# Performance work log

Hardware: AMD Instinct MI355X
Metric: run time of the kernel (lower is better)

The kernel has to match this reference:

```python
import jax, jax.numpy as jnp
import numpy as np

MARGIN = 0.3


def setup_inputs() -> dict:
    key = jax.random.key(0)
    k1, k2 = jax.random.split(key)
    N, D = 8192, 128
    embeddings = jax.random.normal(k1, (N, D), dtype=jnp.float32)
    labels = jax.random.randint(k2, (N,), 0, 512, dtype=jnp.int64)
    return {"embeddings": embeddings, "labels": labels}


def _pairwise_dist(x):
    # Euclidean cdist via squared-norm expansion; safe sqrt (zero grad at d==0).
    sq_norms = jnp.sum(x * x, axis=-1)  # [N]
    sq = sq_norms[:, None] + sq_norms[None, :] - 2.0 * (x @ x.T)  # [N, N]
    sq = jnp.maximum(sq, 0.0)
    safe = jnp.where(sq > 0.0, sq, 1.0)
    return jnp.where(sq > 0.0, jnp.sqrt(safe), 0.0)


def reference(embeddings, labels):
    d = _pairwise_dist(embeddings)  # [N, N]
    same = labels[:, None] == labels[None, :]
    eye = jnp.eye(labels.shape[0], dtype=bool)
    pos_mask = same & ~eye
    neg_mask = ~same

    inf = jnp.float32(jnp.inf)
    hardest_pos = jnp.max(jnp.where(pos_mask, d, -inf), axis=1)  # [N]
    hardest_neg = jnp.min(jnp.where(neg_mask, d, inf), axis=1)   # [N]

    valid = jnp.any(pos_mask, axis=1) & jnp.any(neg_mask, axis=1)
    per_row = jax.nn.relu(hardest_pos - hardest_neg + MARGIN)
    per_row = jnp.where(valid, per_row, 0.0)
    count = jnp.sum(valid)
    return jnp.where(count > 0, jnp.sum(per_row) / jnp.maximum(count, 1), 0.0)
```

## Files before the change

kernel.cpp:

```cpp
#include <hip/hip_runtime.h>
#include <hip/hip_fp16.h>

#define N 8192
#define D 128
#define MARGIN 0.3f

typedef __fp16 half_t;
typedef __attribute__((ext_vector_type(8))) __fp16 half8;
typedef __attribute__((ext_vector_type(4))) float f32x4;

__global__ void triplet_prep(const float* __restrict__ x,
                             half_t* __restrict__ xh,
                             float* __restrict__ norms,
                             float* __restrict__ gacc) {
    const int gt = blockIdx.x * 256 + threadIdx.x;
    if (gt < 3) gacc[gt] = 0.f;
    const int row  = gt >> 6;
    const int lane = gt & 63;
    const float* rp = x + (size_t)row * D;
    float a0 = rp[lane], a1 = rp[lane + 64];
    xh[(size_t)row * D + lane]      = (half_t)a0;
    xh[(size_t)row * D + lane + 64] = (half_t)a1;
    float s = fmaf(a0, a0, a1 * a1);
#pragma unroll
    for (int o = 32; o > 0; o >>= 1) s += __shfl_xor(s, o);
    if (lane == 0) norms[row] = s;
}


#define PF(BN, LJN, NJN, SN) {                                          \
    const int jn = colbase + (SN) * 16 + lcol;                          \
    const half_t* bp = xh + (size_t)jn * D + lrow * 8;                  \
    BN[0] = *(const half8*)bp;                                          \
    BN[1] = *(const half8*)(bp + 32);                                   \
    BN[2] = *(const half8*)(bp + 64);                                   \
    BN[3] = *(const half8*)(bp + 96);                                   \
    LJN = labels[jn];                                                   \
    NJN = norms[jn];                                                    \
}

#define POISON(ACC) {                                                   \
    _Pragma("unroll")                                                   \
    for (int rg = 0; rg < 4; ++rg)                                      \
        ACC[rg] = (diagl && rg == drg) ? 1e30f : ACC[rg];               \
}

#define EPI(ACC, FI, LJC, NJC) {                                        \
    _Pragma("unroll")                                                   \
    for (int rg = 0; rg < 4; ++rg) {                                    \
        float c = fmaf(-2.f, ACC[rg], (NJC));                           \
        bool same = (li[(FI) * 4 + rg] == (LJC));                       \
        mpos[(FI)*4+rg] = same ? fmaxf(mpos[(FI)*4+rg], c) : mpos[(FI)*4+rg]; \
        mneg[(FI)*4+rg] = same ? mneg[(FI)*4+rg] : fminf(mneg[(FI)*4+rg], c); \
    }                                                                   \
}

#define COMP(BC, LJC, NJC, S) {                                         \
    f32x4 a0 = {0,0,0,0}, a1 = {0,0,0,0}, a2 = {0,0,0,0}, a3 = {0,0,0,0}; \
    __builtin_amdgcn_s_setprio(1);                                      \
    _Pragma("unroll")                                                   \
    for (int ks = 0; ks < 4; ++ks) {                                    \
        a0 = __builtin_amdgcn_mfma_f32_16x16x32_f16(af[0][ks], BC[ks], a0, 0, 0, 0); \
        a1 = __builtin_amdgcn_mfma_f32_16x16x32_f16(af[1][ks], BC[ks], a1, 0, 0, 0); \
        a2 = __builtin_amdgcn_mfma_f32_16x16x32_f16(af[2][ks], BC[ks], a2, 0, 0, 0); \
        a3 = __builtin_amdgcn_mfma_f32_16x16x32_f16(af[3][ks], BC[ks], a3, 0, 0, 0); \
    }                                                                   \
    __builtin_amdgcn_s_setprio(0);                                      \
    const int dj = colbase + (S) * 16 - rowbase;                        \
    if (dj == 0)       POISON(a0)                                       \
    else if (dj == 16) POISON(a1)                                       \
    else if (dj == 32) POISON(a2)                                       \
    else if (dj == 48) POISON(a3)                                       \
    EPI(a0, 0, LJC, NJC)                                                \
    EPI(a1, 1, LJC, NJC)                                                \
    EPI(a2, 2, LJC, NJC)                                                \
    EPI(a3, 3, LJC, NJC)                                                \
}

__launch_bounds__(256, 2)
__global__ void triplet_main(const half_t* __restrict__ xh,
                             const float* __restrict__ norms,
                             const int* __restrict__ labels,
                             float* __restrict__ ppos,
                             float* __restrict__ pneg) {
    const int tid   = threadIdx.x;
    const int lane  = tid & 63;
    const int gw    = blockIdx.x * 4 + (tid >> 6);
    const int rowg  = gw >> 4;
    const int chunk = gw & 15;
    const int lrow  = lane >> 4;
    const int lcol  = lane & 15;
    const int rowbase = rowg * 64;
    const int colbase = chunk * 512;
    const bool diagl = (lrow == (lcol >> 2));
    const int  drg   = lcol & 3;

    half8 af[4][4];
#pragma unroll
    for (int fi = 0; fi < 4; ++fi) {
        const half_t* ap = xh + (size_t)(rowbase + fi * 16 + lcol) * D + lrow * 8;
#pragma unroll
        for (int ks = 0; ks < 4; ++ks)
            af[fi][ks] = *(const half8*)(ap + ks * 32);
    }

    const int ibase = rowbase + lrow * 4;
    int li[16];
#pragma unroll
    for (int fi = 0; fi < 4; ++fi)
#pragma unroll
        for (int rg = 0; rg < 4; ++rg)
            li[fi * 4 + rg] = labels[ibase + fi * 16 + rg];

    float mpos[16], mneg[16];
#pragma unroll
    for (int r = 0; r < 16; ++r) { mpos[r] = -1e38f; mneg[r] = 1e38f; }

    half8 b0[4], b1[4], b2[4];
    int lj0, lj1, lj2; float nj0, nj1, nj2;
    PF(b0, lj0, nj0, 0)
    PF(b1, lj1, nj1, 1)
    for (int s = 0; s < 30; s += 3) {
        PF(b2, lj2, nj2, s + 2)
        COMP(b0, lj0, nj0, s)
        PF(b0, lj0, nj0, s + 3)
        COMP(b1, lj1, nj1, s + 1)
        PF(b1, lj1, nj1, s + 4)
        COMP(b2, lj2, nj2, s + 2)
    }
    COMP(b0, lj0, nj0, 30)
    COMP(b1, lj1, nj1, 31)

#pragma unroll
    for (int o = 1; o < 16; o <<= 1) {
#pragma unroll
        for (int r = 0; r < 16; ++r) {
            mpos[r] = fmaxf(mpos[r], __shfl_xor(mpos[r], o));
            mneg[r] = fminf(mneg[r], __shfl_xor(mneg[r], o));
        }
    }
    if (lcol == 0) {
#pragma unroll
        for (int fi = 0; fi < 4; ++fi)
#pragma unroll
            for (int rg = 0; rg < 4; ++rg) {
                int row = ibase + fi * 16 + rg;
                ppos[(size_t)row * 16 + chunk] = mpos[fi * 4 + rg];
                pneg[(size_t)row * 16 + chunk] = mneg[fi * 4 + rg];
            }
    }
}

__global__ void triplet_reduce(const float* __restrict__ ppos,
                               const float* __restrict__ pneg,
                               const float* __restrict__ norms,
                               float* __restrict__ gacc,
                               float* __restrict__ out) {
    __shared__ float ss[256];
    __shared__ float sc[256];
    const int tid = threadIdx.x;
    const int r   = blockIdx.x * 256 + tid;
    float mp = -1e38f, mn = 1e38f;
    const f32x4* pp = (const f32x4*)(ppos + (size_t)r * 16);
    const f32x4* pn = (const f32x4*)(pneg + (size_t)r * 16);
#pragma unroll
    for (int s4 = 0; s4 < 4; ++s4) {
        f32x4 a = pp[s4], b = pn[s4];
#pragma unroll
        for (int e = 0; e < 4; ++e) { mp = fmaxf(mp, a[e]); mn = fminf(mn, b[e]); }
    }
    float ni = norms[r];
    bool valid = (mp > -1e37f) && (mn < 1e37f);
    float hp = sqrtf(fmaxf(ni + mp, 0.f));
    float hn = sqrtf(fmaxf(ni + mn, 0.f));
    float pr = fmaxf(hp - hn + MARGIN, 0.f);
    ss[tid] = valid ? pr : 0.f;
    sc[tid] = valid ? 1.f : 0.f;
    __syncthreads();
    for (int o = 128; o > 0; o >>= 1) {
        if (tid < o) { ss[tid] += ss[tid + o]; sc[tid] += sc[tid + o]; }
        __syncthreads();
    }
    if (tid == 0) {
        atomicAdd(&gacc[0], ss[0]);
        atomicAdd(&gacc[1], sc[0]);
        __threadfence();
        unsigned* ticket = (unsigned*)(gacc + 2);
        unsigned old = atomicAdd(ticket, 1u);
        if (old == gridDim.x - 1) {
            float s = atomicAdd(&gacc[0], 0.f);
            float c = atomicAdd(&gacc[1], 0.f);
            out[0] = (c > 0.f) ? (s / c) : 0.f;
        }
    }
}

extern "C" void kernel_launch(void* const* d_in, const int* in_sizes, int n_in,
                              void* d_out, int out_size, void* d_ws, size_t ws_size,
                              hipStream_t stream) {
    const float* x      = (const float*)d_in[0];
    const int*   labels = (const int*)d_in[1];
    float*       out    = (float*)d_out;

    char*   ws    = (char*)d_ws;
    half_t* xh    = (half_t*)ws;
    float*  norms = (float*)(ws + (size_t)N * D * sizeof(half_t));
    float*  ppos  = norms + N;
    float*  pneg  = ppos + (size_t)N * 16;
    float*  gacc  = pneg + (size_t)N * 16;

    triplet_prep  <<<N / 4,   256, 0, stream>>>(x, xh, norms, gacc);
    triplet_main  <<<512,     256, 0, stream>>>(xh, norms, labels, ppos, pneg);
    triplet_reduce<<<N / 256, 256, 0, stream>>>(ppos, pneg, norms, gacc, out);
}
```

Before: 55.07 us.

## Pack fp16 operands in MFMA fragment order and fold norm into accumulator init

Adds a pack kernel that writes the fp16 copy of the embeddings tiled in the per-lane MFMA fragment order, so each B-fragment load is fully contiguous across the wavefront instead of strided by row. The A fragments are pre-scaled by -2 and the column norm is used as the initial MFMA accumulator, which removes the per-element fma from the epilogue. The diagonal poison value is flipped to stay consistent with the new sign. This adds a fourth kernel launch and splits the prep work into two passes over the input.

Result: faster. 48.50 us (-11.9%).

```diff
diff --git a/kernel.cpp b/kernel.cpp
--- a/kernel.cpp
+++ b/kernel.cpp
@@ -9,8 +9,7 @@
 typedef __attribute__((ext_vector_type(8))) __fp16 half8;
 typedef __attribute__((ext_vector_type(4))) float f32x4;
 
-__global__ void triplet_prep(const float* __restrict__ x,
-                             half_t* __restrict__ xh,
+__global__ void triplet_norm(const float* __restrict__ x,
                              float* __restrict__ norms,
                              float* __restrict__ gacc) {
     const int gt = blockIdx.x * 256 + threadIdx.x;
@@ -19,22 +18,34 @@
     const int lane = gt & 63;
     const float* rp = x + (size_t)row * D;
     float a0 = rp[lane], a1 = rp[lane + 64];
-    xh[(size_t)row * D + lane]      = (half_t)a0;
-    xh[(size_t)row * D + lane + 64] = (half_t)a1;
     float s = fmaf(a0, a0, a1 * a1);
 #pragma unroll
     for (int o = 32; o > 0; o >>= 1) s += __shfl_xor(s, o);
     if (lane == 0) norms[row] = s;
 }
 
+__global__ void triplet_pack(const float* __restrict__ x,
+                             half_t* __restrict__ xp) {
+    const int gid = blockIdx.x * 256 + threadIdx.x;
+    const int t   = gid >> 8;
+    const int i   = gid & 255;
+    const int row = t * 16 + (i & 15);
+    const int k0  = ((i >> 4) & 15) * 8;
+    const float* rp = x + (size_t)row * D + k0;
+    half_t v[8];
+#pragma unroll
+    for (int e = 0; e < 8; ++e) v[e] = (half_t)rp[e];
+    *(half8*)(xp + (size_t)gid * 8) = *(const half8*)v;
+}
+
 
 #define PF(BN, LJN, NJN, SN) {                                          \
+    const half_t* bp = xp + ((size_t)(colbase >> 4) + (SN)) * 2048 + lane * 8; \
+    BN[0] = *(const half8*)bp;                                          \
+    BN[1] = *(const half8*)(bp + 512);                                  \
+    BN[2] = *(const half8*)(bp + 1024);                                 \
+    BN[3] = *(const half8*)(bp + 1536);                                 \
     const int jn = colbase + (SN) * 16 + lcol;                          \
-    const half_t* bp = xh + (size_t)jn * D + lrow * 8;                  \
-    BN[0] = *(const half8*)bp;                                          \
-    BN[1] = *(const half8*)(bp + 32);                                   \
-    BN[2] = *(const half8*)(bp + 64);                                   \
-    BN[3] = *(const half8*)(bp + 96);                                   \
     LJN = labels[jn];                                                   \
     NJN = norms[jn];                                                    \
 }
@@ -42,13 +53,13 @@
 #define POISON(ACC) {                                                   \
     _Pragma("unroll")                                                   \
     for (int rg = 0; rg < 4; ++rg)                                      \
-        ACC[rg] = (diagl && rg == drg) ? 1e30f : ACC[rg];               \
-}
-
-#define EPI(ACC, FI, LJC, NJC) {                                        \
+        ACC[rg] = (diagl && rg == drg) ? -1e30f : ACC[rg];              \
+}
+
+#define EPI(ACC, FI, LJC) {                                             \
     _Pragma("unroll")                                                   \
     for (int rg = 0; rg < 4; ++rg) {                                    \
-        float c = fmaf(-2.f, ACC[rg], (NJC));                           \
+        float c = ACC[rg];                                              \
         bool same = (li[(FI) * 4 + rg] == (LJC));                       \
         mpos[(FI)*4+rg] = same ? fmaxf(mpos[(FI)*4+rg], c) : mpos[(FI)*4+rg]; \
         mneg[(FI)*4+rg] = same ? mneg[(FI)*4+rg] : fminf(mneg[(FI)*4+rg], c); \
@@ -56,10 +67,14 @@
 }
 
 #define COMP(BC, LJC, NJC, S) {                                         \
-    f32x4 a0 = {0,0,0,0}, a1 = {0,0,0,0}, a2 = {0,0,0,0}, a3 = {0,0,0,0}; \
+    f32x4 njq = {NJC, NJC, NJC, NJC};                                   \
     __builtin_amdgcn_s_setprio(1);                                      \
+    f32x4 a0 = __builtin_amdgcn_mfma_f32_16x16x32_f16(af[0][0], BC[0], njq, 0, 0, 0); \
+    f32x4 a1 = __builtin_amdgcn_mfma_f32_16x16x32_f16(af[1][0], BC[0], njq, 0, 0, 0); \
+    f32x4 a2 = __builtin_amdgcn_mfma_f32_16x16x32_f16(af[2][0], BC[0], njq, 0, 0, 0); \
+    f32x4 a3 = __builtin_amdgcn_mfma_f32_16x16x32_f16(af[3][0], BC[0], njq, 0, 0, 0); \
     _Pragma("unroll")                                                   \
-    for (int ks = 0; ks < 4; ++ks) {                                    \
+    for (int ks = 1; ks < 4; ++ks) {                                    \
         a0 = __builtin_amdgcn_mfma_f32_16x16x32_f16(af[0][ks], BC[ks], a0, 0, 0, 0); \
         a1 = __builtin_amdgcn_mfma_f32_16x16x32_f16(af[1][ks], BC[ks], a1, 0, 0, 0); \
         a2 = __builtin_amdgcn_mfma_f32_16x16x32_f16(af[2][ks], BC[ks], a2, 0, 0, 0); \
@@ -71,14 +86,14 @@
     else if (dj == 16) POISON(a1)                                       \
     else if (dj == 32) POISON(a2)                                       \
     else if (dj == 48) POISON(a3)                                       \
-    EPI(a0, 0, LJC, NJC)                                                \
-    EPI(a1, 1, LJC, NJC)                                                \
-    EPI(a2, 2, LJC, NJC)                                                \
-    EPI(a3, 3, LJC, NJC)                                                \
+    EPI(a0, 0, LJC)                                                     \
+    EPI(a1, 1, LJC)                                                     \
+    EPI(a2, 2, LJC)                                                     \
+    EPI(a3, 3, LJC)                                                     \
 }
 
 __launch_bounds__(256, 2)
-__global__ void triplet_main(const half_t* __restrict__ xh,
+__global__ void triplet_main(const half_t* __restrict__ xp,
                              const float* __restrict__ norms,
                              const int* __restrict__ labels,
                              float* __restrict__ ppos,
@@ -98,10 +113,10 @@
     half8 af[4][4];
 #pragma unroll
     for (int fi = 0; fi < 4; ++fi) {
-        const half_t* ap = xh + (size_t)(rowbase + fi * 16 + lcol) * D + lrow * 8;
+        const half_t* ap = xp + ((size_t)(rowbase >> 4) + fi) * 2048 + lane * 8;
 #pragma unroll
         for (int ks = 0; ks < 4; ++ks)
-            af[fi][ks] = *(const half8*)(ap + ks * 32);
+            af[fi][ks] = *(const half8*)(ap + ks * 512) * (half_t)(-2.0f);
     }
 
     const int ibase = rowbase + lrow * 4;
@@ -203,13 +218,14 @@
     float*       out    = (float*)d_out;
 
     char*   ws    = (char*)d_ws;
-    half_t* xh    = (half_t*)ws;
+    half_t* xp    = (half_t*)ws;
     float*  norms = (float*)(ws + (size_t)N * D * sizeof(half_t));
     float*  ppos  = norms + N;
     float*  pneg  = ppos + (size_t)N * 16;
     float*  gacc  = pneg + (size_t)N * 16;
 
-    triplet_prep  <<<N / 4,   256, 0, stream>>>(x, xh, norms, gacc);
-    triplet_main  <<<512,     256, 0, stream>>>(xh, norms, labels, ppos, pneg);
-    triplet_reduce<<<N / 256, 256, 0, stream>>>(ppos, pneg, norms, gacc, out);
-}
+    triplet_norm  <<<N / 4,        256, 0, stream>>>(x, norms, gacc);
+    triplet_pack  <<<N * 16 / 256, 256, 0, stream>>>(x, xp);
+    triplet_main  <<<512,          256, 0, stream>>>(xp, norms, labels, ppos, pneg);
+    triplet_reduce<<<N / 256,      256, 0, stream>>>(ppos, pneg, norms, gacc, out);
+}
```
